# Kernel optimization log

Hardware: AMD Instinct MI355X
Metric: run time of the kernel (lower is better)

Reference implementation:

```python
import jax, jax.numpy as jnp
import numpy as np

N = 50000      # nodes
E = 800000     # edges (avg degree 16)
DIN = 128      # input_dim
DG = 128       # gnn_dim
DCLS = 128     # cls_dim
DOUT = 10      # output_dim
LMDA = 1.0     # rw_lmda
P_DROP = 0.5


def setup_inputs() -> dict:
    key = jax.random.key(0)
    ks = jax.random.split(key, 12)
    x = jax.random.normal(ks[0], (N, DIN), jnp.float32)
    edge_index = jax.random.randint(ks[1], (2, E), 0, N, dtype=jnp.int64)
    edge_weight = jax.random.uniform(ks[2], (E,), jnp.float32)
    def glorot(k, shape):
        lim = np.sqrt(6.0 / (shape[0] + shape[1])).astype(np.float32)
        return jax.random.uniform(k, shape, jnp.float32, -lim, lim)
    return dict(
        x=x, edge_index=edge_index, edge_weight=edge_weight,
        W_lin_in=glorot(ks[3], (DIN, DG)), b_lin_in=jnp.zeros((DG,), jnp.float32),
        W_agg_in=glorot(ks[4], (DG + DIN, DG)), b_agg_in=jnp.zeros((DG,), jnp.float32),
        W_lin_h=glorot(ks[5], (DG, DG)), b_lin_h=jnp.zeros((DG,), jnp.float32),
        W_agg_h=glorot(ks[6], (2 * DG, DG)), b_agg_h=jnp.zeros((DG,), jnp.float32),
        W_mlp1=glorot(ks[7], (DG, DCLS)), b_mlp1=jnp.zeros((DCLS,), jnp.float32),
        W_mlp2=glorot(ks[8], (DCLS, DOUT)), b_mlp2=jnp.zeros((DOUT,), jnp.float32),
    )


def _gs_layer(x, row, col, ew, inv_cnt, W_lin, b_lin, W_agg, b_agg):
    # GS_reweight: message = (1-lmda)*lin(x_j) + lmda*ew*lin(x_j), mean-aggregated
    # at row (flow='target_to_source': gather from col, scatter to row).
    h = x @ W_lin + b_lin                      # [N, DG] (lin before gather == lin(x_j))
    hj = h[col]                                # [E, DG] gather
    m = (1.0 - LMDA) * hj + LMDA * (ew[:, None] * hj)
    agg = jax.ops.segment_sum(m, row, num_segments=N) * inv_cnt[:, None]  # mean
    out = jnp.concatenate([agg, x], axis=-1) @ W_agg + b_agg              # update()
    return jax.nn.relu(out)


def _dropout(x, k):
    mask = jax.random.bernoulli(k, 1.0 - P_DROP, x.shape)
    return jnp.where(mask, x / (1.0 - P_DROP), 0.0)


def reference(x, edge_index, edge_weight,
              W_lin_in, b_lin_in, W_agg_in, b_agg_in,
              W_lin_h, b_lin_h, W_agg_h, b_agg_h,
              W_mlp1, b_mlp1, W_mlp2, b_mlp2):
    row, col = edge_index[0], edge_index[1]
    cnt = jax.ops.segment_sum(jnp.ones((E,), x.dtype), row, num_segments=N)
    inv_cnt = 1.0 / jnp.maximum(cnt, 1.0)     # scatter_mean: empty rows -> 0
    dk = jax.random.split(jax.random.key(42), 3)
    h = _gs_layer(x, row, col, edge_weight, inv_cnt, W_lin_in, b_lin_in, W_agg_in, b_agg_in)
    h = _dropout(jax.nn.relu(h), dk[0])       # relu is idempotent after update's relu
    for i in range(2):                        # layers 2,3 share prop_hidden weights
        h = _gs_layer(h, row, col, edge_weight, inv_cnt, W_lin_h, b_lin_h, W_agg_h, b_agg_h)
        h = _dropout(jax.nn.relu(h), dk[i + 1])
    y = jax.nn.relu(h @ W_mlp1 + b_mlp1) @ W_mlp2 + b_mlp2  # cls_layers=2, bn=False
    return (h, y)
```

## Files before the change

### kernel.cpp

```cpp
#include <hip/hip_runtime.h>
#include <cstdint>
#include <cstddef>


#define N_NODES 50000
#define N_EDGES 800000
#define DGN 128
#define DOUT 10
#define NELEM (N_NODES * DGN)
#define NMASKW (NELEM / 64)
#define NBINS 391
#define TILE 4096
#define NTILES ((N_EDGES + TILE - 1) / TILE)
#define GBF ((N_NODES + 63) / 64)
#define MK_BLOCKS 25000
#define AB_BLOCKS ((N_NODES + 7) / 8)

#define XB_BLK 6250
#define HI_BLK NTILES
#define WC_BLK 128
#define TR_BLK 192
#define R0 XB_BLK
#define R1 (R0 + HI_BLK)
#define R2 (R1 + WC_BLK)
#define R3 (R2 + TR_BLK)
#define MEGA_BLOCKS (R3 + 1)

typedef __attribute__((ext_vector_type(8))) short bf16x8;
typedef __attribute__((ext_vector_type(4))) float f32x4;

__host__ __device__ static inline unsigned short f2bf(float f) {
  union { float f; unsigned u; } c; c.f = f;
  unsigned u = c.u;
  return (unsigned short)((u + 0x7fffu + ((u >> 16) & 1u)) >> 16);
}
__device__ static inline float bflo(unsigned u) { return __uint_as_float(u << 16); }
__device__ static inline float bfhi(unsigned u) { return __uint_as_float(u & 0xffff0000u); }
__device__ static inline float bf2f(unsigned short h) {
  return __uint_as_float(((unsigned)h) << 16);
}

__host__ __device__ static inline void tf2x32(unsigned k0, unsigned k1,
                                              unsigned c0, unsigned c1,
                                              unsigned& o0, unsigned& o1) {
  unsigned ks2 = k0 ^ k1 ^ 0x1BD11BDAu;
  unsigned x0 = c0 + k0;
  unsigned x1 = c1 + k1;
#define TFR(r) { x0 += x1; x1 = (x1 << (r)) | (x1 >> (32 - (r))); x1 ^= x0; }
  TFR(13) TFR(15) TFR(26) TFR(6)
  x0 += k1;  x1 += ks2 + 1u;
  TFR(17) TFR(29) TFR(16) TFR(24)
  x0 += ks2; x1 += k0 + 2u;
  TFR(13) TFR(15) TFR(26) TFR(6)
  x0 += k0;  x1 += k1 + 3u;
  TFR(17) TFR(29) TFR(16) TFR(24)
  x0 += k1;  x1 += ks2 + 4u;
  TFR(13) TFR(15) TFR(26) TFR(6)
  x0 += ks2; x1 += k0 + 5u;
#undef TFR
  o0 = x0; o1 = x1;
}

__device__ static inline void mask_chunk(unsigned long long* __restrict__ gm,
                                         int i, unsigned k0, unsigned k1) {
  unsigned o0, o1;
  tf2x32(k0, k1, 0u, (unsigned)i, o0, o1);
  unsigned long long b = __ballot(((o0 ^ o1) >> 31) == 0u);
  if ((threadIdx.x & 63) == 0) gm[i >> 6] = b;
}

__global__ __launch_bounds__(256) void mega_kernel(
    const float* __restrict__ x, unsigned short* __restrict__ xb,
    const int* __restrict__ ei, int* __restrict__ chist,
    const float* __restrict__ Wli, const float* __restrict__ Wai,
    const float* __restrict__ Wlh, const float* __restrict__ Wah,
    const float* __restrict__ Wm1,
    const float* __restrict__ bli, const float* __restrict__ blh,
    unsigned short* __restrict__ Tai, unsigned short* __restrict__ Tah,
    unsigned short* __restrict__ Tm1,
    float* __restrict__ bvi, float* __restrict__ bvh) {
  __shared__ int h[NBINS];
  const int b = blockIdx.x;
  const int tid = threadIdx.x;

  if (b < R0) {
    int g = b * 256 + tid;
    float4 v = ((const float4*)x)[g];
    ushort4 o;
    o.x = f2bf(v.x); o.y = f2bf(v.y); o.z = f2bf(v.z); o.w = f2bf(v.w);
    ((ushort4*)xb)[g] = o;
  } else if (b < R1) {
    for (int i = tid; i < NBINS; i += 256) h[i] = 0;
    __syncthreads();
    const int e0 = (b - R0) * TILE;
#pragma unroll 4
    for (int j = 0; j < TILE; j += 256) {
      int e = e0 + j + tid;
      if (e < N_EDGES) {
        int r = ei[e];
        r = (r < 0) ? 0 : (r >= N_NODES ? N_NODES - 1 : r);
        atomicAdd(&h[r >> 7], 1);
      }
    }
    __syncthreads();
    for (int i = tid; i < NBINS; i += 256)
      if (h[i]) atomicAdd(&chist[i], h[i]);
  } else if (b < R2) {
    int idx = (b - R1) * 256 + tid;
    int n = idx & 127;
    int k = (idx >> 7) & 127;
    int m = idx >> 14;
    const float* Wl = m ? Wlh : Wli;
    const float* Wa = m ? Wah : Wai;
    unsigned short* T = m ? Tah : Tai;
    float acc = 0.0f;
#pragma unroll 8
    for (int j = 0; j < 128; ++j)
      acc += Wl[k * 128 + j] * Wa[j * 128 + n];
    T[n * 256 + k] = f2bf(acc);
  } else if (b < R3) {
    int j = (b - R2) * 256 + tid;
    if (j < 16384) {
      int kk = j & 127, n = j >> 7;
      Tai[n * 256 + 128 + kk] = f2bf(Wai[(size_t)(128 + kk) * 128 + n]);
    } else if (j < 32768) {
      int q = j - 16384;
      int kk = q & 127, n = q >> 7;
      Tah[n * 256 + 128 + kk] = f2bf(Wah[(size_t)(128 + kk) * 128 + n]);
    } else {
      int q = j - 32768;
      int k = q & 127, n = q >> 7;
      Tm1[n * 128 + k] = f2bf(Wm1[(size_t)k * 128 + n]);
    }
  } else {
    int n = tid & 127;
    const float* bl = (tid < 128) ? bli : blh;
    const float* Wa = (tid < 128) ? Wai : Wah;
    float acc = 0.0f;
    for (int j = 0; j < 128; ++j) acc += bl[j] * Wa[j * 128 + n];
    if (tid < 128) bvi[n] = acc; else bvh[n] = acc;
  }
}

__global__ __launch_bounds__(512) void prefix_kernel(const int* __restrict__ chist,
                                                     int* __restrict__ cbase,
                                                     int* __restrict__ ccursor,
                                                     int* __restrict__ rowptr) {
  __shared__ int s[512];
  const int t = threadIdx.x;
  int v = (t < NBINS) ? chist[t] : 0;
  s[t] = v;
  __syncthreads();
  for (int off = 1; off < 512; off <<= 1) {
    int tv = (t >= off) ? s[t - off] : 0;
    __syncthreads();
    s[t] += tv;
    __syncthreads();
  }
  if (t <= NBINS) {
    int ex = (t == 0) ? 0 : s[t - 1];
    cbase[t] = ex;
    if (t < NBINS) ccursor[t] = ex;
  }
  if (t == 0) rowptr[N_NODES] = N_EDGES;
}

__global__ __launch_bounds__(256) void scatter_kernel(const int* __restrict__ ei,
                                                      const float* __restrict__ ew,
                                                      int* __restrict__ ccursor,
                                                      uint2* __restrict__ pk,
                                                      unsigned long long* __restrict__ mg0,
                                                      unsigned k00, unsigned k01) {
  if (blockIdx.x >= NTILES) {
    mask_chunk(mg0, (blockIdx.x - NTILES) * 256 + threadIdx.x, k00, k01);
    return;
  }
  __shared__ uint2 st[TILE];
  __shared__ unsigned short sbin[TILE];
  __shared__ int h[NBINS];
  __shared__ int base[NBINS];
  __shared__ int gbase[NBINS];
  __shared__ int cur[NBINS];
  __shared__ int sc[512];
  const int tid = threadIdx.x;
  const int e0 = blockIdx.x * TILE;
  const int nt = (N_EDGES - e0 < TILE) ? (N_EDGES - e0) : TILE;

  for (int i = tid; i < NBINS; i += 256) { h[i] = 0; cur[i] = 0; }
  __syncthreads();
  for (int j = tid; j < nt; j += 256) {
    int r = ei[e0 + j];
    r = (r < 0) ? 0 : (r >= N_NODES ? N_NODES - 1 : r);
    atomicAdd(&h[r >> 7], 1);
  }
  __syncthreads();
  sc[tid] = (tid < NBINS) ? h[tid] : 0;
  sc[tid + 256] = (tid + 256 < NBINS) ? h[tid + 256] : 0;
  __syncthreads();
  for (int off = 1; off < 512; off <<= 1) {
    int a0 = (tid >= off) ? sc[tid - off] : 0;
    int a1 = (tid + 256 >= off) ? sc[tid + 256 - off] : 0;
    __syncthreads();
    sc[tid] += a0; sc[tid + 256] += a1;
    __syncthreads();
  }
  if (tid < NBINS) {
    base[tid] = sc[tid] - h[tid];
    if (h[tid]) gbase[tid] = atomicAdd(&ccursor[tid], h[tid]);
  }
  if (tid + 256 < NBINS) {
    base[tid + 256] = sc[tid + 256] - h[tid + 256];
    if (h[tid + 256]) gbase[tid + 256] = atomicAdd(&ccursor[tid + 256], h[tid + 256]);
  }
  __syncthreads();
  for (int j = tid; j < nt; j += 256) {
    int r = ei[e0 + j];
    r = (r < 0) ? 0 : (r >= N_NODES ? N_NODES - 1 : r);
    int c = ei[N_EDGES + e0 + j];
    c = (c < 0) ? 0 : (c >= N_NODES ? N_NODES - 1 : c);
    int bb = r >> 7;
    int slot = base[bb] + atomicAdd(&cur[bb], 1);
    uint2 p;
    p.x = ((unsigned)r << 16) | (unsigned)c;
    p.y = __float_as_uint(ew[e0 + j]);
    st[slot] = p;
    sbin[slot] = (unsigned short)bb;
  }
  __syncthreads();
  for (int j = tid; j < nt; j += 256) {
    int bb = sbin[j];
    pk[gbase[bb] + (j - base[bb])] = st[j];
  }
}

__global__ __launch_bounds__(256) void place_kernel(const int* __restrict__ cbase,
                                                    const uint2* __restrict__ pk,
                                                    uint2* __restrict__ csr,
                                                    int* __restrict__ rowptr,
                                                    float* __restrict__ invc) {
  __shared__ int lcnt[128];
  __shared__ int lpre[128];
  __shared__ int lcur[128];
  __shared__ int sc[128];
  const int b = blockIdx.x;
  const int tid = threadIdx.x;
  const int cb = cbase[b];
  const int n = cbase[b + 1] - cb;
  const int r0 = b << 7;
  const int nr = (N_NODES - r0 < 128) ? (N_NODES - r0) : 128;

  if (tid < 128) { lcnt[tid] = 0; lcur[tid] = 0; }
  __syncthreads();
  for (int i = tid; i < n; i += 256) {
    int r7 = (int)(pk[cb + i].x >> 16) - r0;
    atomicAdd(&lcnt[r7], 1);
  }
  __syncthreads();
  if (tid < 128) sc[tid] = lcnt[tid];
  __syncthreads();
  for (int off = 1; off < 128; off <<= 1) {
    int tv = (tid >= off && tid < 128) ? sc[tid - off] : 0;
    __syncthreads();
    if (tid < 128) sc[tid] += tv;
    __syncthreads();
  }
  if (tid < 128) lpre[tid] = sc[tid] - lcnt[tid];
  __syncthreads();
  if (tid < nr) {
    rowptr[r0 + tid] = cb + lpre[tid];
    int c = lcnt[tid];
    invc[r0 + tid] = 1.0f / (float)(c > 1 ? c : 1);
  }
  for (int i = tid; i < n; i += 256) {
    uint2 p = pk[cb + i];
    int r7 = (int)(p.x >> 16) - r0;
    int slot = cb + lpre[r7] + atomicAdd(&lcur[r7], 1);
    uint2 o;
    o.x = p.x & 0xFFFFu;
    o.y = p.y;
    csr[slot] = o;
  }
}

__global__ __launch_bounds__(256) void agg_kernel(const unsigned short* __restrict__ hlin,
                                                  const int* __restrict__ rowptr,
                                                  const uint2* __restrict__ csr,
                                                  const float* __restrict__ invc,
                                                  unsigned short* __restrict__ agg,
                                                  float* __restrict__ swout) {
  const int lane = threadIdx.x & 63;
  const int wid = threadIdx.x >> 6;
  const int wrow = lane >> 5;
  const int slot = (lane >> 4) & 1;
  const int cg = lane & 15;
  const int r = blockIdx.x * 8 + wid * 2 + wrow;
  const int start = rowptr[r];
  const int num = rowptr[r + 1] - start;
  const uint4* __restrict__ H = (const uint4*)hlin;

  float a[8] = {0.f, 0.f, 0.f, 0.f, 0.f, 0.f, 0.f, 0.f};
  float ws = 0.f;
  for (int e = 0; e < num; e += 16) {
#pragma unroll
    for (int j = 0; j < 8; ++j) {
      int idx = e + j * 2 + slot;
      bool ok = idx < num;
      int idxc = ok ? idx : (num - 1);
      uint2 q = csr[start + idxc];
      float w = ok ? __uint_as_float(q.y) : 0.0f;
      uint4 p = H[(size_t)q.x * 16 + cg];
      ws += w;
      a[0] += w * bflo(p.x); a[1] += w * bfhi(p.x);
      a[2] += w * bflo(p.y); a[3] += w * bfhi(p.y);
      a[4] += w * bflo(p.z); a[5] += w * bfhi(p.z);
      a[6] += w * bflo(p.w); a[7] += w * bfhi(p.w);
    }
  }
#pragma unroll
  for (int k = 0; k < 8; ++k) a[k] += __shfl_xor(a[k], 16);
  ws += __shfl_xor(ws, 16);
  const float s = invc[r];
  if (slot == 0) {
    uint4 o;
    o.x = (unsigned)f2bf(a[0] * s) | ((unsigned)f2bf(a[1] * s) << 16);
    o.y = (unsigned)f2bf(a[2] * s) | ((unsigned)f2bf(a[3] * s) << 16);
    o.z = (unsigned)f2bf(a[4] * s) | ((unsigned)f2bf(a[5] * s) << 16);
    o.w = (unsigned)f2bf(a[6] * s) | ((unsigned)f2bf(a[7] * s) << 16);
    ((uint4*)agg)[(size_t)r * 16 + cg] = o;
    if (swout && cg == 0) swout[r] = ws * s;
  }
}

template <bool WF32, bool MASKGEN>
__global__ __launch_bounds__(256) void layer_gemm(
    const unsigned short* __restrict__ Agg, const unsigned short* __restrict__ Hin,
    const unsigned short* __restrict__ Wt,
    const float* __restrict__ bvec, const float* __restrict__ bagg,
    const float* __restrict__ sw,
    const unsigned long long* __restrict__ maskw,
    float* __restrict__ outf, unsigned short* __restrict__ outb,
    unsigned long long* __restrict__ gm, unsigned gk0, unsigned gk1) {
  if (MASKGEN && blockIdx.x >= GBF) {
    mask_chunk(gm, (blockIdx.x - GBF) * 256 + threadIdx.x, gk0, gk1);
    return;
  }
  constexpr int LS = 72;
  __shared__ unsigned short Als[64 * LS];
  __shared__ unsigned short Bls[128 * LS];
  const int tid = threadIdx.x;
  const int m0 = blockIdx.x * 64;
  const int lane = tid & 63;
  const int wid = tid >> 6;
  const int wm = (wid >> 1) * 32;
  const int wn = (wid & 1) * 64;
  const int ln = lane & 15;
  const int lh = lane >> 4;
  const int sArow = tid >> 2;
  const int sAk = (tid & 3) * 16;
  const int sBcol = tid >> 1;
  const int sBk = (tid & 1) * 32;
  int arow = m0 + sArow;
  if (arow >= N_NODES) arow = N_NODES - 1;

  f32x4 acc[2][4];
#pragma unroll
  for (int i = 0; i < 2; ++i)
#pragma unroll
    for (int j = 0; j < 4; ++j)
#pragma unroll
      for (int r = 0; r < 4; ++r) acc[i][j][r] = 0.0f;

  for (int kb = 0; kb < 256; kb += 64) {
    const unsigned short* Asrc = (kb < 128) ? Agg : Hin;
    const unsigned short* ap = Asrc + (size_t)arow * 128 + (kb & 127) + sAk;
    unsigned short* al = &Als[sArow * LS + sAk];
    *(uint4*)(al + 0) = *(const uint4*)(ap + 0);
    *(uint4*)(al + 8) = *(const uint4*)(ap + 8);
    const unsigned short* bp = Wt + (size_t)sBcol * 256 + kb + sBk;
    unsigned short* bl = &Bls[sBcol * LS + sBk];
    *(uint4*)(bl + 0)  = *(const uint4*)(bp + 0);
    *(uint4*)(bl + 8)  = *(const uint4*)(bp + 8);
    *(uint4*)(bl + 16) = *(const uint4*)(bp + 16);
    *(uint4*)(bl + 24) = *(const uint4*)(bp + 24);
    __syncthreads();
#pragma unroll
    for (int ks = 0; ks < 64; ks += 32) {
      bf16x8 af[2], bfr[4];
#pragma unroll
      for (int i = 0; i < 2; ++i)
        af[i] = *(const bf16x8*)&Als[(wm + i * 16 + ln) * LS + ks + lh * 8];
#pragma unroll
      for (int j = 0; j < 4; ++j)
        bfr[j] = *(const bf16x8*)&Bls[(wn + j * 16 + ln) * LS + ks + lh * 8];
#pragma unroll
      for (int i = 0; i < 2; ++i)
#pragma unroll
        for (int j = 0; j < 4; ++j)
          acc[i][j] = __builtin_amdgcn_mfma_f32_16x16x32_bf16(af[i], bfr[j], acc[i][j], 0, 0, 0);
    }
    __syncthreads();
  }

  const int lm = lane >> 4;
  float bc[4], b2[4];
#pragma unroll
  for (int j = 0; j < 4; ++j) {
    int col = wn + j * 16 + ln;
    bc[j] = bvec[col];
    b2[j] = bagg[col];
  }
#pragma unroll
  for (int i = 0; i < 2; ++i) {
    const int lr0 = wm + i * 16 + lm * 4;
#pragma unroll
    for (int r = 0; r < 4; ++r) {
      const int row = m0 + lr0 + r;
      if (row >= N_NODES) continue;
      const float swr = sw[row];
      const unsigned long long mw = maskw[(size_t)row * 2 + (wn >> 6)];
#pragma unroll
      for (int j = 0; j < 4; ++j) {
        const int col = wn + j * 16 + ln;
        float v = acc[i][j][r] + swr * bc[j] + b2[j];
        v = fmaxf(v, 0.0f);
        v = ((mw >> (col & 63)) & 1ull) ? 2.0f * v : 0.0f;
        if (WF32) outf[(size_t)row * DGN + col] = v;
        outb[(size_t)row * DGN + col] = f2bf(v);
      }
    }
  }
}

__global__ __launch_bounds__(256) void mlp_gemm(
    const unsigned short* __restrict__ A0,
    const unsigned short* __restrict__ Wt,
    const float* __restrict__ b1,
    const float* __restrict__ W2, const float* __restrict__ b2,
    float* __restrict__ y) {
  constexpr int LS = 72;
  constexpr int LT = 132;
  __shared__ unsigned short Als[64 * LS];
  __shared__ unsigned short Bls[128 * LS];
  __shared__ unsigned short tT[64 * LT];
  __shared__ float Ws[128 * DOUT];
  __shared__ float bs[DOUT];
  const int tid = threadIdx.x;
  const int m0 = blockIdx.x * 64;
  const int lane = tid & 63;
  const int wid = tid >> 6;
  const int wm = (wid >> 1) * 32;
  const int wn = (wid & 1) * 64;
  const int ln = lane & 15;
  const int lh = lane >> 4;
  const int sArow = tid >> 2;
  const int sAk = (tid & 3) * 16;
  const int sBcol = tid >> 1;
  const int sBk = (tid & 1) * 32;
  int arow = m0 + sArow;
  if (arow >= N_NODES) arow = N_NODES - 1;

  for (int i = tid; i < 128 * DOUT; i += 256) Ws[i] = W2[i];
  if (tid < DOUT) bs[tid] = b2[tid];

  f32x4 acc[2][4];
#pragma unroll
  for (int i = 0; i < 2; ++i)
#pragma unroll
    for (int j = 0; j < 4; ++j)
#pragma unroll
      for (int r = 0; r < 4; ++r) acc[i][j][r] = 0.0f;

  for (int kb = 0; kb < 128; kb += 64) {
    const unsigned short* ap = A0 + (size_t)arow * 128 + kb + sAk;
    unsigned short* al = &Als[sArow * LS + sAk];
    *(uint4*)(al + 0) = *(const uint4*)(ap + 0);
    *(uint4*)(al + 8) = *(const uint4*)(ap + 8);
    const unsigned short* bp = Wt + (size_t)sBcol * 128 + kb + sBk;
    unsigned short* bl = &Bls[sBcol * LS + sBk];
    *(uint4*)(bl + 0)  = *(const uint4*)(bp + 0);
    *(uint4*)(bl + 8)  = *(const uint4*)(bp + 8);
    *(uint4*)(bl + 16) = *(const uint4*)(bp + 16);
    *(uint4*)(bl + 24) = *(const uint4*)(bp + 24);
    __syncthreads();
#pragma unroll
    for (int ks = 0; ks < 64; ks += 32) {
      bf16x8 af[2], bfr[4];
#pragma unroll
      for (int i = 0; i < 2; ++i)
        af[i] = *(const bf16x8*)&Als[(wm + i * 16 + ln) * LS + ks + lh * 8];
#pragma unroll
      for (int j = 0; j < 4; ++j)
        bfr[j] = *(const bf16x8*)&Bls[(wn + j * 16 + ln) * LS + ks + lh * 8];
#pragma unroll
      for (int i = 0; i < 2; ++i)
#pragma unroll
        for (int j = 0; j < 4; ++j)
          acc[i][j] = __builtin_amdgcn_mfma_f32_16x16x32_bf16(af[i], bfr[j], acc[i][j], 0, 0, 0);
    }
    __syncthreads();
  }

  const int lm = lane >> 4;
  float bcol[4];
#pragma unroll
  for (int j = 0; j < 4; ++j) bcol[j] = b1[wn + j * 16 + ln];
#pragma unroll
  for (int i = 0; i < 2; ++i) {
    const int lr0 = wm + i * 16 + lm * 4;
#pragma unroll
    for (int r = 0; r < 4; ++r) {
      const int lr = lr0 + r;
#pragma unroll
      for (int j = 0; j < 4; ++j) {
        const int col = wn + j * 16 + ln;
        float v = fmaxf(acc[i][j][r] + bcol[j], 0.0f);
        tT[lr * LT + col] = f2bf(v);
      }
    }
  }
  __syncthreads();

  if (tid < 64) {
    int row = m0 + tid;
    if (row < N_NODES) {
      float a2[DOUT];
#pragma unroll
      for (int c = 0; c < DOUT; ++c) a2[c] = bs[c];
      const unsigned short* tr = &tT[tid * LT];
#pragma unroll 8
      for (int k = 0; k < 128; ++k) {
        float tv = bf2f(tr[k]);
        const float* wr = &Ws[k * DOUT];
#pragma unroll
        for (int c = 0; c < DOUT; ++c) a2[c] += tv * wr[c];
      }
      float* yp = y + (size_t)row * DOUT;
#pragma unroll
      for (int c = 0; c < DOUT; ++c) yp[c] = a2[c];
    }
  }
}

extern "C" void kernel_launch(void* const* d_in, const int* in_sizes, int n_in,
                              void* d_out, int out_size, void* d_ws, size_t ws_size,
                              hipStream_t stream) {
  const float* x        = (const float*)d_in[0];
  const int*   ei       = (const int*)d_in[1];
  const float* ew       = (const float*)d_in[2];
  const float* W_lin_in = (const float*)d_in[3];
  const float* b_lin_in = (const float*)d_in[4];
  const float* W_agg_in = (const float*)d_in[5];
  const float* b_agg_in = (const float*)d_in[6];
  const float* W_lin_h  = (const float*)d_in[7];
  const float* b_lin_h  = (const float*)d_in[8];
  const float* W_agg_h  = (const float*)d_in[9];
  const float* b_agg_h  = (const float*)d_in[10];
  const float* W_mlp1   = (const float*)d_in[11];
  const float* b_mlp1   = (const float*)d_in[12];
  const float* W_mlp2   = (const float*)d_in[13];
  const float* b_mlp2   = (const float*)d_in[14];

  float* hout = (float*)d_out;
  float* yout = hout + (size_t)NELEM;

  char* p = (char*)d_ws;
  auto alloc = [&](size_t bytes) {
    char* q = p;
    p += (bytes + 255) & ~(size_t)255;
    return q;
  };
  int*   chist   = (int*)alloc((size_t)(NBINS + 1) * 4);
  int*   cbase   = (int*)alloc((size_t)(NBINS + 1) * 4);
  int*   ccursor = (int*)alloc((size_t)NBINS * 4);
  int*   rowptr  = (int*)alloc((size_t)(N_NODES + 1) * 4);
  float* invc    = (float*)alloc((size_t)N_NODES * 4);
  float* swv     = (float*)alloc((size_t)N_NODES * 4);
  uint2* pk      = (uint2*)alloc((size_t)N_EDGES * 8);
  uint2* csr     = (uint2*)alloc((size_t)N_EDGES * 8);
  unsigned short* xb   = (unsigned short*)alloc((size_t)NELEM * 2);
  unsigned short* aggb = (unsigned short*)alloc((size_t)NELEM * 2);
  unsigned short* hA   = (unsigned short*)alloc((size_t)NELEM * 2);
  unsigned short* hB   = (unsigned short*)alloc((size_t)NELEM * 2);
  unsigned long long* mw0 = (unsigned long long*)alloc((size_t)NMASKW * 8);
  unsigned long long* mw1 = (unsigned long long*)alloc((size_t)NMASKW * 8);
  unsigned long long* mw2 = (unsigned long long*)alloc((size_t)NMASKW * 8);
  unsigned short* Tai = (unsigned short*)alloc(32768 * 2);
  unsigned short* Tah = (unsigned short*)alloc(32768 * 2);
  unsigned short* Tm1 = (unsigned short*)alloc(16384 * 2);
  float* bvi = (float*)alloc(128 * 4);
  float* bvh = (float*)alloc(128 * 4);

  unsigned dk[3][2];
  for (unsigned i = 0; i < 3; ++i) tf2x32(0u, 42u, 0u, i, dk[i][0], dk[i][1]);

  hipMemsetAsync(chist, 0, (size_t)(NBINS + 1) * 4, stream);
  mega_kernel<<<MEGA_BLOCKS, 256, 0, stream>>>(
      x, xb, ei, chist, W_lin_in, W_agg_in, W_lin_h, W_agg_h, W_mlp1,
      b_lin_in, b_lin_h, Tai, Tah, Tm1, bvi, bvh);

  prefix_kernel<<<1, 512, 0, stream>>>(chist, cbase, ccursor, rowptr);
  scatter_kernel<<<NTILES + MK_BLOCKS, 256, 0, stream>>>(
      ei, ew, ccursor, pk, mw0, dk[0][0], dk[0][1]);
  place_kernel<<<NBINS, 256, 0, stream>>>(cbase, pk, csr, rowptr, invc);

  agg_kernel<<<AB_BLOCKS, 256, 0, stream>>>(xb, rowptr, csr, invc, aggb, swv);
  layer_gemm<false, true><<<GBF + MK_BLOCKS, 256, 0, stream>>>(
      aggb, xb, Tai, bvi, b_agg_in, swv, mw0, nullptr, hA,
      mw1, dk[1][0], dk[1][1]);

  agg_kernel<<<AB_BLOCKS, 256, 0, stream>>>(hA, rowptr, csr, invc, aggb, nullptr);
  layer_gemm<false, true><<<GBF + MK_BLOCKS, 256, 0, stream>>>(
      aggb, hA, Tah, bvh, b_agg_h, swv, mw1, nullptr, hB,
      mw2, dk[2][0], dk[2][1]);

  agg_kernel<<<AB_BLOCKS, 256, 0, stream>>>(hB, rowptr, csr, invc, aggb, nullptr);
  layer_gemm<true, false><<<GBF, 256, 0, stream>>>(
      aggb, hB, Tah, bvh, b_agg_h, swv, mw2, hout, hA,
      nullptr, 0, 0);

  mlp_gemm<<<GBF, 256, 0, stream>>>(hA, Tm1, b_mlp1, W_mlp2, b_mlp2, yout);
}
```

Measured before the change: 328.8 us.

## Remove prefix kernel; recompute bin scan per block and fold prep into scatter

Removes the single-block prefix-scan kernel. Each scatter and place block now recomputes the 391-bin exclusive scan from the global histogram in shared memory. The ccursor counters become zero-based offsets added to the scanned base. The bf16 conversion of x and the weight-precombination work move from the old mega kernel into extra blocks of the scatter kernel, leaving a small histogram-only kernel in front. This saves one launch and one serialized tiny kernel, at the cost of a redundant 512-wide scan in every scatter and place block.

```diff
diff --git a/kernel.cpp b/kernel.cpp
--- a/kernel.cpp
+++ b/kernel.cpp
@@ -16,15 +16,15 @@
 #define MK_BLOCKS 25000
 #define AB_BLOCKS ((N_NODES + 7) / 8)
 
-#define XB_BLK 6250
-#define HI_BLK NTILES
-#define WC_BLK 128
-#define TR_BLK 192
-#define R0 XB_BLK
-#define R1 (R0 + HI_BLK)
-#define R2 (R1 + WC_BLK)
-#define R3 (R2 + TR_BLK)
-#define MEGA_BLOCKS (R3 + 1)
+#define S_XB 6250
+#define S_WC 128
+#define S_TR 192
+#define SR0 NTILES
+#define SR1 (SR0 + MK_BLOCKS)
+#define SR2 (SR1 + S_XB)
+#define SR3 (SR2 + S_WC)
+#define SR4 (SR3 + S_TR)
+#define SCATTER_BLOCKS (SR4 + 1)
 
 typedef __attribute__((ext_vector_type(8))) short bf16x8;
 typedef __attribute__((ext_vector_type(4))) float f32x4;
@@ -69,9 +69,33 @@
   if ((threadIdx.x & 63) == 0) gm[i >> 6] = b;
 }
 
-__global__ __launch_bounds__(256) void mega_kernel(
+__global__ __launch_bounds__(256) void hist_kernel(const int* __restrict__ ei,
+                                                   int* __restrict__ chist) {
+  __shared__ int h[NBINS];
+  const int tid = threadIdx.x;
+  for (int i = tid; i < NBINS; i += 256) h[i] = 0;
+  __syncthreads();
+  const int e0 = blockIdx.x * TILE;
+#pragma unroll 4
+  for (int j = 0; j < TILE; j += 256) {
+    int e = e0 + j + tid;
+    if (e < N_EDGES) {
+      int r = ei[e];
+      r = (r < 0) ? 0 : (r >= N_NODES ? N_NODES - 1 : r);
+      atomicAdd(&h[r >> 7], 1);
+    }
+  }
+  __syncthreads();
+  for (int i = tid; i < NBINS; i += 256)
+    if (h[i]) atomicAdd(&chist[i], h[i]);
+}
+
+__global__ __launch_bounds__(256) void scatter_kernel(
+    const int* __restrict__ ei, const float* __restrict__ ew,
+    const int* __restrict__ chist, int* __restrict__ ccursor,
+    uint2* __restrict__ pk,
+    unsigned long long* __restrict__ mg0, unsigned k00, unsigned k01,
     const float* __restrict__ x, unsigned short* __restrict__ xb,
-    const int* __restrict__ ei, int* __restrict__ chist,
     const float* __restrict__ Wli, const float* __restrict__ Wai,
     const float* __restrict__ Wlh, const float* __restrict__ Wah,
     const float* __restrict__ Wm1,
@@ -79,102 +103,55 @@
     unsigned short* __restrict__ Tai, unsigned short* __restrict__ Tah,
     unsigned short* __restrict__ Tm1,
     float* __restrict__ bvi, float* __restrict__ bvh) {
-  __shared__ int h[NBINS];
-  const int b = blockIdx.x;
   const int tid = threadIdx.x;
-
-  if (b < R0) {
-    int g = b * 256 + tid;
-    float4 v = ((const float4*)x)[g];
-    ushort4 o;
-    o.x = f2bf(v.x); o.y = f2bf(v.y); o.z = f2bf(v.z); o.w = f2bf(v.w);
-    ((ushort4*)xb)[g] = o;
-  } else if (b < R1) {
-    for (int i = tid; i < NBINS; i += 256) h[i] = 0;
-    __syncthreads();
-    const int e0 = (b - R0) * TILE;
-#pragma unroll 4
-    for (int j = 0; j < TILE; j += 256) {
-      int e = e0 + j + tid;
-      if (e < N_EDGES) {
-        int r = ei[e];
-        r = (r < 0) ? 0 : (r >= N_NODES ? N_NODES - 1 : r);
-        atomicAdd(&h[r >> 7], 1);
+  if (blockIdx.x >= SR0) {
+    const int rb = blockIdx.x;
+    if (rb < SR1) {
+      mask_chunk(mg0, (rb - SR0) * 256 + tid, k00, k01);
+    } else if (rb < SR2) {
+      int g = (rb - SR1) * 256 + tid;
+      float4 v = ((const float4*)x)[g];
+      ushort4 o;
+      o.x = f2bf(v.x); o.y = f2bf(v.y); o.z = f2bf(v.z); o.w = f2bf(v.w);
+      ((ushort4*)xb)[g] = o;
+    } else if (rb < SR3) {
+      int idx = (rb - SR2) * 256 + tid;
+      int n = idx & 127;
+      int k = (idx >> 7) & 127;
+      int m = idx >> 14;
+      const float* Wl = m ? Wlh : Wli;
+      const float* Wa = m ? Wah : Wai;
+      unsigned short* T = m ? Tah : Tai;
+      float acc = 0.0f;
+#pragma unroll 8
+      for (int j = 0; j < 128; ++j)
+        acc += Wl[k * 128 + j] * Wa[j * 128 + n];
+      T[n * 256 + k] = f2bf(acc);
+    } else if (rb < SR4) {
+      int j = (rb - SR3) * 256 + tid;
+      if (j < 16384) {
+        int kk = j & 127, n = j >> 7;
+        Tai[n * 256 + 128 + kk] = f2bf(Wai[(size_t)(128 + kk) * 128 + n]);
+      } else if (j < 32768) {
+        int q = j - 16384;
+        int kk = q & 127, n = q >> 7;
+        Tah[n * 256 + 128 + kk] = f2bf(Wah[(size_t)(128 + kk) * 128 + n]);
+      } else {
+        int q = j - 32768;
+        int k = q & 127, n = q >> 7;
+        Tm1[n * 128 + k] = f2bf(Wm1[(size_t)k * 128 + n]);
       }
-    }
-    __syncthreads();
-    for (int i = tid; i < NBINS; i += 256)
-      if (h[i]) atomicAdd(&chist[i], h[i]);
-  } else if (b < R2) {
-    int idx = (b - R1) * 256 + tid;
-    int n = idx & 127;
-    int k = (idx >> 7) & 127;
-    int m = idx >> 14;
-    const float* Wl = m ? Wlh : Wli;
-    const float* Wa = m ? Wah : Wai;
-    unsigned short* T = m ? Tah : Tai;
-    float acc = 0.0f;
-#pragma unroll 8
-    for (int j = 0; j < 128; ++j)
-      acc += Wl[k * 128 + j] * Wa[j * 128 + n];
-    T[n * 256 + k] = f2bf(acc);
-  } else if (b < R3) {
-    int j = (b - R2) * 256 + tid;
-    if (j < 16384) {
-      int kk = j & 127, n = j >> 7;
-      Tai[n * 256 + 128 + kk] = f2bf(Wai[(size_t)(128 + kk) * 128 + n]);
-    } else if (j < 32768) {
-      int q = j - 16384;
-      int kk = q & 127, n = q >> 7;
-      Tah[n * 256 + 128 + kk] = f2bf(Wah[(size_t)(128 + kk) * 128 + n]);
     } else {
-      int q = j - 32768;
-      int k = q & 127, n = q >> 7;
-      Tm1[n * 128 + k] = f2bf(Wm1[(size_t)k * 128 + n]);
-    }
-  } else {
-    int n = tid & 127;
-    const float* bl = (tid < 128) ? bli : blh;
-    const float* Wa = (tid < 128) ? Wai : Wah;
-    float acc = 0.0f;
-    for (int j = 0; j < 128; ++j) acc += bl[j] * Wa[j * 128 + n];
-    if (tid < 128) bvi[n] = acc; else bvh[n] = acc;
-  }
-}
-
-__global__ __launch_bounds__(512) void prefix_kernel(const int* __restrict__ chist,
-                                                     int* __restrict__ cbase,
-                                                     int* __restrict__ ccursor,
-                                                     int* __restrict__ rowptr) {
-  __shared__ int s[512];
-  const int t = threadIdx.x;
-  int v = (t < NBINS) ? chist[t] : 0;
-  s[t] = v;
-  __syncthreads();
-  for (int off = 1; off < 512; off <<= 1) {
-    int tv = (t >= off) ? s[t - off] : 0;
-    __syncthreads();
-    s[t] += tv;
-    __syncthreads();
-  }
-  if (t <= NBINS) {
-    int ex = (t == 0) ? 0 : s[t - 1];
-    cbase[t] = ex;
-    if (t < NBINS) ccursor[t] = ex;
-  }
-  if (t == 0) rowptr[N_NODES] = N_EDGES;
-}
-
-__global__ __launch_bounds__(256) void scatter_kernel(const int* __restrict__ ei,
-                                                      const float* __restrict__ ew,
-                                                      int* __restrict__ ccursor,
-                                                      uint2* __restrict__ pk,
-                                                      unsigned long long* __restrict__ mg0,
-                                                      unsigned k00, unsigned k01) {
-  if (blockIdx.x >= NTILES) {
-    mask_chunk(mg0, (blockIdx.x - NTILES) * 256 + threadIdx.x, k00, k01);
+      int n = tid & 127;
+      const float* bl = (tid < 128) ? bli : blh;
+      const float* Wa = (tid < 128) ? Wai : Wah;
+      float acc = 0.0f;
+      for (int j = 0; j < 128; ++j) acc += bl[j] * Wa[j * 128 + n];
+      if (tid < 128) bvi[n] = acc; else bvh[n] = acc;
+    }
     return;
   }
+
   __shared__ uint2 st[TILE];
   __shared__ unsigned short sbin[TILE];
   __shared__ int h[NBINS];
@@ -182,12 +159,21 @@
   __shared__ int gbase[NBINS];
   __shared__ int cur[NBINS];
   __shared__ int sc[512];
-  const int tid = threadIdx.x;
+  __shared__ int gsc[512];
   const int e0 = blockIdx.x * TILE;
   const int nt = (N_EDGES - e0 < TILE) ? (N_EDGES - e0) : TILE;
 
   for (int i = tid; i < NBINS; i += 256) { h[i] = 0; cur[i] = 0; }
-  __syncthreads();
+  gsc[tid] = (tid < NBINS) ? chist[tid] : 0;
+  gsc[tid + 256] = (tid + 256 < NBINS) ? chist[tid + 256] : 0;
+  __syncthreads();
+  for (int off = 1; off < 512; off <<= 1) {
+    int a0 = (tid >= off) ? gsc[tid - off] : 0;
+    int a1 = (tid + 256 >= off) ? gsc[tid + 256 - off] : 0;
+    __syncthreads();
+    gsc[tid] += a0; gsc[tid + 256] += a1;
+    __syncthreads();
+  }
   for (int j = tid; j < nt; j += 256) {
     int r = ei[e0 + j];
     r = (r < 0) ? 0 : (r >= N_NODES ? N_NODES - 1 : r);
@@ -206,11 +192,13 @@
   }
   if (tid < NBINS) {
     base[tid] = sc[tid] - h[tid];
-    if (h[tid]) gbase[tid] = atomicAdd(&ccursor[tid], h[tid]);
+    if (h[tid])
+      gbase[tid] = ((tid == 0) ? 0 : gsc[tid - 1]) + atomicAdd(&ccursor[tid], h[tid]);
   }
   if (tid + 256 < NBINS) {
     base[tid + 256] = sc[tid + 256] - h[tid + 256];
-    if (h[tid + 256]) gbase[tid + 256] = atomicAdd(&ccursor[tid + 256], h[tid + 256]);
+    if (h[tid + 256])
+      gbase[tid + 256] = gsc[tid + 255] + atomicAdd(&ccursor[tid + 256], h[tid + 256]);
   }
   __syncthreads();
   for (int j = tid; j < nt; j += 256) {
@@ -233,7 +221,7 @@
   }
 }
 
-__global__ __launch_bounds__(256) void place_kernel(const int* __restrict__ cbase,
+__global__ __launch_bounds__(256) void place_kernel(const int* __restrict__ chist,
                                                     const uint2* __restrict__ pk,
                                                     uint2* __restrict__ csr,
                                                     int* __restrict__ rowptr,
@@ -242,15 +230,27 @@
   __shared__ int lpre[128];
   __shared__ int lcur[128];
   __shared__ int sc[128];
+  __shared__ int gsc[512];
   const int b = blockIdx.x;
   const int tid = threadIdx.x;
-  const int cb = cbase[b];
-  const int n = cbase[b + 1] - cb;
+
+  gsc[tid] = (tid < NBINS) ? chist[tid] : 0;
+  gsc[tid + 256] = (tid + 256 < NBINS) ? chist[tid + 256] : 0;
+  if (tid < 128) { lcnt[tid] = 0; lcur[tid] = 0; }
+  __syncthreads();
+  for (int off = 1; off < 512; off <<= 1) {
+    int a0 = (tid >= off) ? gsc[tid - off] : 0;
+    int a1 = (tid + 256 >= off) ? gsc[tid + 256 - off] : 0;
+    __syncthreads();
+    gsc[tid] += a0; gsc[tid + 256] += a1;
+    __syncthreads();
+  }
+  const int cb = (b == 0) ? 0 : gsc[b - 1];
+  const int n = chist[b];
   const int r0 = b << 7;
   const int nr = (N_NODES - r0 < 128) ? (N_NODES - r0) : 128;
-
-  if (tid < 128) { lcnt[tid] = 0; lcur[tid] = 0; }
-  __syncthreads();
+  if (b == 0 && tid == 0) rowptr[N_NODES] = N_EDGES;
+
   for (int i = tid; i < n; i += 256) {
     int r7 = (int)(pk[cb + i].x >> 16) - r0;
     atomicAdd(&lcnt[r7], 1);
@@ -569,9 +569,9 @@
     p += (bytes + 255) & ~(size_t)255;
     return q;
   };
-  int*   chist   = (int*)alloc((size_t)(NBINS + 1) * 4);
-  int*   cbase   = (int*)alloc((size_t)(NBINS + 1) * 4);
-  int*   ccursor = (int*)alloc((size_t)NBINS * 4);
+  int*   csrmeta = (int*)alloc((size_t)(2 * NBINS + 2) * 4);
+  int*   chist   = csrmeta;
+  int*   ccursor = csrmeta + NBINS + 1;
   int*   rowptr  = (int*)alloc((size_t)(N_NODES + 1) * 4);
   float* invc    = (float*)alloc((size_t)N_NODES * 4);
   float* swv     = (float*)alloc((size_t)N_NODES * 4);
@@ -593,15 +593,13 @@
   unsigned dk[3][2];
   for (unsigned i = 0; i < 3; ++i) tf2x32(0u, 42u, 0u, i, dk[i][0], dk[i][1]);
 
-  hipMemsetAsync(chist, 0, (size_t)(NBINS + 1) * 4, stream);
-  mega_kernel<<<MEGA_BLOCKS, 256, 0, stream>>>(
-      x, xb, ei, chist, W_lin_in, W_agg_in, W_lin_h, W_agg_h, W_mlp1,
+  hipMemsetAsync(csrmeta, 0, (size_t)(2 * NBINS + 2) * 4, stream);
+  hist_kernel<<<NTILES, 256, 0, stream>>>(ei, chist);
+  scatter_kernel<<<SCATTER_BLOCKS, 256, 0, stream>>>(
+      ei, ew, chist, ccursor, pk, mw0, dk[0][0], dk[0][1],
+      x, xb, W_lin_in, W_agg_in, W_lin_h, W_agg_h, W_mlp1,
       b_lin_in, b_lin_h, Tai, Tah, Tm1, bvi, bvh);
-
-  prefix_kernel<<<1, 512, 0, stream>>>(chist, cbase, ccursor, rowptr);
-  scatter_kernel<<<NTILES + MK_BLOCKS, 256, 0, stream>>>(
-      ei, ew, ccursor, pk, mw0, dk[0][0], dk[0][1]);
-  place_kernel<<<NBINS, 256, 0, stream>>>(cbase, pk, csr, rowptr, invc);
+  place_kernel<<<NBINS, 256, 0, stream>>>(chist, pk, csr, rowptr, invc);
 
   agg_kernel<<<AB_BLOCKS, 256, 0, stream>>>(xb, rowptr, csr, invc, aggb, swv);
   layer_gemm<false, true><<<GBF + MK_BLOCKS, 256, 0, stream>>>(
```

After: 336.1 us. 1.02x slower.
